# Optimization experiments

Measured on AMD Instinct MI355X. Metric: run time of the kernel, lower is better.

## Reference

```python
import jax, jax.numpy as jnp
import numpy as np

N_BASE = 4          # len('NACGT'[1:])
STATE_LEN = 5
S = N_BASE ** STATE_LEN   # 1024 states
NZ = N_BASE + 1           # 5 transitions per state
T_STEPS = 800
BATCH = 32


def _build_idx():
    # idx[i] = [i, 0*256 + i//4, 1*256 + i//4, 2*256 + i//4, 3*256 + i//4]
    i = np.arange(S)
    trans = np.stack([j * (S // N_BASE) + i // N_BASE for j in range(N_BASE)], axis=1)
    idx = np.concatenate([i[:, None], trans], axis=1).astype(np.int64)      # (S, NZ)
    # transposed transition structure (stable sort: duplicates grouped deterministically)
    idx_T = np.argsort(idx.ravel(), kind='stable').reshape(S, NZ)
    idx_T_div = idx_T // NZ
    return jnp.asarray(idx), jnp.asarray(idx_T), jnp.asarray(idx_T_div)


def _scan(Ms, idx, v0):
    """Log-semiring recurrence: alpha[t+1] = logsumexp(Ms[t] + alpha[t][:, idx], -1).
    Ms: (T, N, S, NZ); idx: (S, NZ); v0: (N, S). Returns (T+1, N, S)."""
    def step(alpha, M):
        nxt = jax.scipy.special.logsumexp(M + alpha[:, idx], axis=-1)  # (N, S)
        return nxt, nxt
    _, alphas = jax.lax.scan(step, v0, Ms)
    return jnp.concatenate([v0[None], alphas], axis=0)


def setup_inputs() -> dict:
    key = jax.random.key(0)
    scores = jax.random.normal(key, (T_STEPS, BATCH, S * NZ), dtype=jnp.float32)
    return {"scores": scores}


def reference(scores):
    idx, idx_T, idx_T_div = _build_idx()
    T, N, _ = scores.shape
    Ms = scores.reshape(T, N, S, NZ)
    v0 = jnp.zeros((N, S), scores.dtype)   # semiring Log.one == 0.0
    # forward scores
    fwd = _scan(Ms, idx, v0)                                   # (T+1, N, S)
    # backward scores: gather transposed transitions, run scan in reverse time
    Ms_T = scores[:, :, idx_T]                                 # (T, N, S, NZ)
    bwd = jnp.flip(_scan(jnp.flip(Ms_T, 0), idx_T_div, v0), 0)  # (T+1, N, S)
    posts = jax.nn.softmax(fwd + bwd, axis=-1)                 # (T+1, N, S)
    return (jnp.swapaxes(scores, 0, 1),
            jnp.swapaxes(bwd, 0, 1),
            jnp.swapaxes(posts, 0, 1))
```

## Files before the change

### kernel.cpp

```cpp
#include <hip/hip_runtime.h>

#define T_STEPS 800
#define NBATCH  32
#define SST     1024
#define ROW     5120

#define SCAN_BLOCKS 64
#define COPY_BLOCKS 1536
#define GRID (SCAN_BLOCKS + COPY_BLOCKS)

__device__ __forceinline__ float lse5(float v0, float v1, float v2, float v3, float v4) {
  float m = fmaxf(fmaxf(fmaxf(v0, v1), fmaxf(v2, v3)), v4);
  float s = __expf(v0 - m) + __expf(v1 - m) + __expf(v2 - m) +
            __expf(v3 - m) + __expf(v4 - m);
  return m + __logf(s);
}

__device__ __forceinline__ void sync_lds() {
  asm volatile("s_waitcnt lgkmcnt(0)" ::: "memory");
  __builtin_amdgcn_s_barrier();
  asm volatile("" ::: "memory");
}

template <int DIR>
__device__ __forceinline__ void prefetch(const float* __restrict__ base, int step, int u,
                                         float* __restrict__ r, float* __restrict__ s) {
  const int t = DIR ? (T_STEPS - 1 - step) : step;
  const float* rp = base + (size_t)t * (NBATCH * ROW);
#pragma unroll
  for (int m = 0; m < 5; ++m)
    *(float4*)&r[4 * m] = *(const float4*)&rp[20 * u + 4 * m];
  if (DIR) {
#pragma unroll
    for (int j = 0; j < 4; ++j) s[j] = rp[5 * u + 1280 * j];
  }
}

template <int DIR>
__device__ void scan_run(const float* __restrict__ scores, float* __restrict__ out,
                         int n, float (*abuf)[SST]) {
  const int u = threadIdx.x;
  const float* base = scores + (size_t)n * ROW;
  float* outn = out + (size_t)n * (T_STEPS + 1) * SST;

  float a[4] = {0.f, 0.f, 0.f, 0.f};

  float v[4][20];
  float s5[4][4];
#pragma unroll
  for (int i = 0; i < 4; ++i) prefetch<DIR>(base, i, u, v[i], s5[i]);

  abuf[0][u] = 0.f; abuf[0][u + 256] = 0.f; abuf[0][u + 512] = 0.f; abuf[0][u + 768] = 0.f;
  {
    const float4 z = {0.f, 0.f, 0.f, 0.f};
    const size_t t0 = DIR ? (size_t)T_STEPS : 0;
    ((float4*)(outn + t0 * SST))[u] = z;
  }
  sync_lds();

  for (int p = 0; p < T_STEPS; p += 4) {
#pragma unroll
    for (int i = 0; i < 4; ++i) {
      const int step = p + i;
      const int cur = step & 1;
      const int nxt = cur ^ 1;

      float4 pv;
      if (DIR == 0) {
        pv.x = abuf[cur][u];
        pv.y = abuf[cur][u + 256];
        pv.z = abuf[cur][u + 512];
        pv.w = abuf[cur][u + 768];
      } else {
        pv = *(const float4*)&abuf[cur][4 * u];
      }

      float na[4];
#pragma unroll
      for (int j = 0; j < 4; ++j) {
        float v0, v1, v2, v3, v4;
        if (DIR == 0) {
          v0 = v[i][5 * j + 0] + a[j];
          v1 = v[i][5 * j + 1] + pv.x;
          v2 = v[i][5 * j + 2] + pv.y;
          v3 = v[i][5 * j + 3] + pv.z;
          v4 = v[i][5 * j + 4] + pv.w;
        } else {
          v0 = s5[i][j]          + a[j];
          v1 = v[i][1 + j + 0]   + pv.x;
          v2 = v[i][1 + j + 5]   + pv.y;
          v3 = v[i][1 + j + 10]  + pv.z;
          v4 = v[i][1 + j + 15]  + pv.w;
        }
        na[j] = lse5(v0, v1, v2, v3, v4);
      }

      if (step + 4 < T_STEPS) prefetch<DIR>(base, step + 4, u, v[i], s5[i]);

      if (DIR == 0) {
        const float4 o = {na[0], na[1], na[2], na[3]};
        ((float4*)(outn + (size_t)(step + 1) * SST))[u] = o;
        *(float4*)&abuf[nxt][4 * u] = o;
      } else {
        const int t = T_STEPS - 1 - step;
#pragma unroll
        for (int j = 0; j < 4; ++j) {
          outn[(size_t)t * SST + u + 256 * j] = na[j];
          abuf[nxt][u + 256 * j] = na[j];
        }
      }
#pragma unroll
      for (int j = 0; j < 4; ++j) a[j] = na[j];

      sync_lds();
    }
  }
}

__global__ __launch_bounds__(256) void mega(const float* __restrict__ scores,
                                            float* __restrict__ out0,
                                            float* __restrict__ bwdo,
                                            float* __restrict__ fposts) {
  __shared__ float abuf[2][SST];
  const int b = blockIdx.x;
  if (b < SCAN_BLOCKS) {
    if (b < NBATCH) scan_run<0>(scores, fposts, b, abuf);
    else            scan_run<1>(scores, bwdo,   b - NBATCH, abuf);
  } else {
    const int tb = b - SCAN_BLOCKS;
    for (int r = tb; r < NBATCH * T_STEPS; r += COPY_BLOCKS) {
      const int t = r / NBATCH, n = r % NBATCH;
      const float4* src = (const float4*)(scores + (size_t)r * ROW);
      float4* dst = (float4*)(out0 + ((size_t)n * T_STEPS + t) * ROW);
#pragma unroll
      for (int i = 0; i < 5; ++i)
        dst[threadIdx.x + 256 * i] = src[threadIdx.x + 256 * i];
    }
  }
}

__global__ __launch_bounds__(256) void posts_kernel(float* __restrict__ fp,
                                                    const float* __restrict__ bp) {
  const int lane = threadIdx.x & 63;
  const int wid  = threadIdx.x >> 6;
  const size_t row = (size_t)blockIdx.x * 4 + wid;
  float* f = fp + row * SST;
  const float* b = bp + row * SST;

  float x[16];
#pragma unroll
  for (int k = 0; k < 4; ++k) {
    const float4 fv = ((const float4*)f)[lane + 64 * k];
    const float4 bv = ((const float4*)b)[lane + 64 * k];
    x[4 * k + 0] = fv.x + bv.x;
    x[4 * k + 1] = fv.y + bv.y;
    x[4 * k + 2] = fv.z + bv.z;
    x[4 * k + 3] = fv.w + bv.w;
  }
  float m = x[0];
#pragma unroll
  for (int j = 1; j < 16; ++j) m = fmaxf(m, x[j]);
#pragma unroll
  for (int off = 32; off >= 1; off >>= 1) m = fmaxf(m, __shfl_xor(m, off));
  float ssum = 0.0f;
#pragma unroll
  for (int j = 0; j < 16; ++j) { x[j] = __expf(x[j] - m); ssum += x[j]; }
#pragma unroll
  for (int off = 32; off >= 1; off >>= 1) ssum += __shfl_xor(ssum, off);
  const float inv = 1.0f / ssum;
#pragma unroll
  for (int k = 0; k < 4; ++k) {
    float4 o;
    o.x = x[4 * k + 0] * inv;
    o.y = x[4 * k + 1] * inv;
    o.z = x[4 * k + 2] * inv;
    o.w = x[4 * k + 3] * inv;
    ((float4*)f)[lane + 64 * k] = o;
  }
}

extern "C" void kernel_launch(void* const* d_in, const int* in_sizes, int n_in,
                              void* d_out, int out_size, void* d_ws, size_t ws_size,
                              hipStream_t stream) {
  (void)in_sizes; (void)n_in; (void)d_ws; (void)ws_size; (void)out_size;
  const float* scores = (const float*)d_in[0];
  float* out = (float*)d_out;
  float* out0   = out;
  float* bwdo   = out + (size_t)NBATCH * T_STEPS * ROW;
  float* fposts = bwdo + (size_t)NBATCH * (T_STEPS + 1) * SST;

  mega<<<GRID, 256, 0, stream>>>(scores, out0, bwdo, fposts);
  posts_kernel<<<(NBATCH * (T_STEPS + 1)) / 4, 256, 0, stream>>>(fposts, bwdo);
}
```

Before: 833.8 us.

## Stage scan score rows into an LDS ring via async global-to-LDS loads

Replaces the per-thread register prefetch of score rows with a five-deep LDS ring buffer filled by global_load_lds DMA instructions, synchronised with explicit vmcnt waits and barriers. The aim is to hide global-memory latency on the serial forward/backward scan and cut register pressure. It adds about 100KB of static LDS per block, which also applies to the copy blocks and limits occupancy, and relies on hand-counted vmcnt thresholds plus an extra barrier per backward step.

New measurement: 694.1 us. 16.7% less time.

```diff
diff --git a/kernel.cpp b/kernel.cpp
--- a/kernel.cpp
+++ b/kernel.cpp
@@ -1,9 +1,11 @@
 #include <hip/hip_runtime.h>
+#include <stdint.h>
 
 #define T_STEPS 800
 #define NBATCH  32
 #define SST     1024
 #define ROW     5120
+#define RING    5
 
 #define SCAN_BLOCKS 64
 #define COPY_BLOCKS 1536
@@ -16,116 +18,162 @@
   return m + __logf(s);
 }
 
-__device__ __forceinline__ void sync_lds() {
+#define WAITVM(N) do { \
+  asm volatile("s_waitcnt vmcnt(" #N ")" ::: "memory"); \
+  __builtin_amdgcn_sched_barrier(0); } while (0)
+
+__device__ __forceinline__ void barrier_lgkm() {
   asm volatile("s_waitcnt lgkmcnt(0)" ::: "memory");
   __builtin_amdgcn_s_barrier();
   asm volatile("" ::: "memory");
 }
 
-template <int DIR>
-__device__ __forceinline__ void prefetch(const float* __restrict__ base, int step, int u,
-                                         float* __restrict__ r, float* __restrict__ s) {
-  const int t = DIR ? (T_STEPS - 1 - step) : step;
-  const float* rp = base + (size_t)t * (NBATCH * ROW);
-#pragma unroll
-  for (int m = 0; m < 5; ++m)
-    *(float4*)&r[4 * m] = *(const float4*)&rp[20 * u + 4 * m];
-  if (DIR) {
-#pragma unroll
-    for (int j = 0; j < 4; ++j) s[j] = rp[5 * u + 1280 * j];
+__device__ __forceinline__ void stage16(const float* g, float* l) {
+  __builtin_amdgcn_global_load_lds(
+      (const __attribute__((address_space(1))) uint32_t*)g,
+      (__attribute__((address_space(3))) uint32_t*)l, 16, 0, 0);
+}
+
+__device__ __forceinline__ void stage_row(const float* __restrict__ rowg,
+                                          float* __restrict__ ldsrow,
+                                          int w, int lane) {
+  const float* src = rowg + 1280 * w + 4 * lane;
+  float* dst = ldsrow + 1280 * w;
+#pragma unroll
+  for (int k = 0; k < 5; ++k) stage16(src + 256 * k, dst + 256 * k);
+}
+
+template <int DIR, int PHASE>
+__device__ __forceinline__ void step_one(int s, int buf, int u, int w, int lane,
+                                         const float* __restrict__ base,
+                                         float* __restrict__ outn,
+                                         float (*ring)[ROW], float (*abuf)[SST],
+                                         float (&a)[4]) {
+  if constexpr (PHASE == 0)      WAITVM(21);
+  else if constexpr (PHASE == 1) { if constexpr (DIR) WAITVM(36); else WAITVM(24); }
+  else                           WAITVM(0);
+
+  if constexpr (DIR) barrier_lgkm();
+
+  const int cur = s & 1;
+  const int nxt = cur ^ 1;
+  const float* rb = ring[buf];
+
+  float4 q[5];
+  const float4* rv = (const float4*)(rb + 20 * u);
+#pragma unroll
+  for (int m = 0; m < 5; ++m) q[m] = rv[m];
+  float fv[20];
+#pragma unroll
+  for (int m = 0; m < 5; ++m) {
+    fv[4 * m + 0] = q[m].x; fv[4 * m + 1] = q[m].y;
+    fv[4 * m + 2] = q[m].z; fv[4 * m + 3] = q[m].w;
+  }
+  float sv[4];
+  if constexpr (DIR) {
+#pragma unroll
+    for (int j = 0; j < 4; ++j) sv[j] = rb[5 * u + 1280 * j];
+  }
+
+  float4 pv;
+  if constexpr (!DIR) {
+    pv.x = abuf[cur][u];
+    pv.y = abuf[cur][u + 256];
+    pv.z = abuf[cur][u + 512];
+    pv.w = abuf[cur][u + 768];
+  } else {
+    pv = *(const float4*)&abuf[cur][4 * u];
+  }
+
+  float na[4];
+#pragma unroll
+  for (int j = 0; j < 4; ++j) {
+    float w0, w1, w2, w3, w4;
+    if constexpr (!DIR) {
+      w0 = fv[5 * j + 0] + a[j];
+      w1 = fv[5 * j + 1] + pv.x;
+      w2 = fv[5 * j + 2] + pv.y;
+      w3 = fv[5 * j + 3] + pv.z;
+      w4 = fv[5 * j + 4] + pv.w;
+    } else {
+      w0 = sv[j]          + a[j];
+      w1 = fv[1 + j + 0]  + pv.x;
+      w2 = fv[1 + j + 5]  + pv.y;
+      w3 = fv[1 + j + 10] + pv.z;
+      w4 = fv[1 + j + 15] + pv.w;
+    }
+    na[j] = lse5(w0, w1, w2, w3, w4);
+    a[j] = na[j];
+  }
+
+  if constexpr (!DIR) {
+    const float4 o = {na[0], na[1], na[2], na[3]};
+    ((float4*)(outn + (size_t)(s + 1) * SST))[u] = o;
+    *(float4*)&abuf[nxt][4 * u] = o;
+  } else {
+    const int t = T_STEPS - 1 - s;
+#pragma unroll
+    for (int j = 0; j < 4; ++j) {
+      outn[(size_t)t * SST + u + 256 * j] = na[j];
+      abuf[nxt][u + 256 * j] = na[j];
+    }
+  }
+
+  barrier_lgkm();
+
+  if constexpr (PHASE != 2) {
+    const int tn = DIR ? (T_STEPS - 1 - (s + RING)) : (s + RING);
+    stage_row(base + (size_t)tn * (NBATCH * ROW), ring[buf], w, lane);
   }
 }
 
 template <int DIR>
 __device__ void scan_run(const float* __restrict__ scores, float* __restrict__ out,
-                         int n, float (*abuf)[SST]) {
+                         int n, float (*ring)[ROW], float (*abuf)[SST]) {
   const int u = threadIdx.x;
+  const int w = u >> 6, lane = u & 63;
   const float* base = scores + (size_t)n * ROW;
   float* outn = out + (size_t)n * (T_STEPS + 1) * SST;
-
   float a[4] = {0.f, 0.f, 0.f, 0.f};
 
-  float v[4][20];
-  float s5[4][4];
-#pragma unroll
-  for (int i = 0; i < 4; ++i) prefetch<DIR>(base, i, u, v[i], s5[i]);
-
-  abuf[0][u] = 0.f; abuf[0][u + 256] = 0.f; abuf[0][u + 512] = 0.f; abuf[0][u + 768] = 0.f;
+#pragma unroll
+  for (int i = 0; i < RING; ++i) {
+    const int t = DIR ? (T_STEPS - 1 - i) : i;
+    stage_row(base + (size_t)t * (NBATCH * ROW), ring[i], w, lane);
+  }
   {
     const float4 z = {0.f, 0.f, 0.f, 0.f};
+    *(float4*)&abuf[0][4 * u] = z;
     const size_t t0 = DIR ? (size_t)T_STEPS : 0;
     ((float4*)(outn + t0 * SST))[u] = z;
   }
-  sync_lds();
-
-  for (int p = 0; p < T_STEPS; p += 4) {
-#pragma unroll
-    for (int i = 0; i < 4; ++i) {
-      const int step = p + i;
-      const int cur = step & 1;
-      const int nxt = cur ^ 1;
-
-      float4 pv;
-      if (DIR == 0) {
-        pv.x = abuf[cur][u];
-        pv.y = abuf[cur][u + 256];
-        pv.z = abuf[cur][u + 512];
-        pv.w = abuf[cur][u + 768];
-      } else {
-        pv = *(const float4*)&abuf[cur][4 * u];
-      }
-
-      float na[4];
-#pragma unroll
-      for (int j = 0; j < 4; ++j) {
-        float v0, v1, v2, v3, v4;
-        if (DIR == 0) {
-          v0 = v[i][5 * j + 0] + a[j];
-          v1 = v[i][5 * j + 1] + pv.x;
-          v2 = v[i][5 * j + 2] + pv.y;
-          v3 = v[i][5 * j + 3] + pv.z;
-          v4 = v[i][5 * j + 4] + pv.w;
-        } else {
-          v0 = s5[i][j]          + a[j];
-          v1 = v[i][1 + j + 0]   + pv.x;
-          v2 = v[i][1 + j + 5]   + pv.y;
-          v3 = v[i][1 + j + 10]  + pv.z;
-          v4 = v[i][1 + j + 15]  + pv.w;
-        }
-        na[j] = lse5(v0, v1, v2, v3, v4);
-      }
-
-      if (step + 4 < T_STEPS) prefetch<DIR>(base, step + 4, u, v[i], s5[i]);
-
-      if (DIR == 0) {
-        const float4 o = {na[0], na[1], na[2], na[3]};
-        ((float4*)(outn + (size_t)(step + 1) * SST))[u] = o;
-        *(float4*)&abuf[nxt][4 * u] = o;
-      } else {
-        const int t = T_STEPS - 1 - step;
-#pragma unroll
-        for (int j = 0; j < 4; ++j) {
-          outn[(size_t)t * SST + u + 256 * j] = na[j];
-          abuf[nxt][u + 256 * j] = na[j];
-        }
-      }
-#pragma unroll
-      for (int j = 0; j < 4; ++j) a[j] = na[j];
-
-      sync_lds();
-    }
-  }
+  barrier_lgkm();
+
+#pragma unroll
+  for (int i = 0; i < RING; ++i)
+    step_one<DIR, 0>(i, i, u, w, lane, base, outn, ring, abuf, a);
+
+  for (int p = RING; p < T_STEPS - RING; p += RING) {
+#pragma unroll
+    for (int i = 0; i < RING; ++i)
+      step_one<DIR, 1>(p + i, i, u, w, lane, base, outn, ring, abuf, a);
+  }
+
+#pragma unroll
+  for (int i = 0; i < RING; ++i)
+    step_one<DIR, 2>(T_STEPS - RING + i, i, u, w, lane, base, outn, ring, abuf, a);
 }
 
 __global__ __launch_bounds__(256) void mega(const float* __restrict__ scores,
                                             float* __restrict__ out0,
                                             float* __restrict__ bwdo,
                                             float* __restrict__ fposts) {
+  __shared__ float ring[RING][ROW];
   __shared__ float abuf[2][SST];
   const int b = blockIdx.x;
   if (b < SCAN_BLOCKS) {
-    if (b < NBATCH) scan_run<0>(scores, fposts, b, abuf);
-    else            scan_run<1>(scores, bwdo,   b - NBATCH, abuf);
+    if (b < NBATCH) scan_run<0>(scores, fposts, b, ring, abuf);
+    else            scan_run<1>(scores, bwdo,   b - NBATCH, ring, abuf);
   } else {
     const int tb = b - SCAN_BLOCKS;
     for (int r = tb; r < NBATCH * T_STEPS; r += COPY_BLOCKS) {
```
